# Performance work log

Hardware: AMD Instinct MI355X
Metric: run time of the kernel (lower is better)

Reference implementation:

```python
import jax, jax.numpy as jnp
import numpy as np


def setup_inputs() -> dict:
    key = jax.random.key(0)
    k1, k2 = jax.random.split(key)
    z = jax.random.normal(k1, (16, 256, 32, 32), dtype=jnp.float32)
    emb = jax.random.normal(k2, (8192, 256), dtype=jnp.float32)
    return {"z": z, "emb": emb}


def reference(z, emb):
    B, C, H, W = z.shape
    # [B,C,H,W] -> [B*H*W, C], distances in fp32 for precision
    z_f = jnp.transpose(z, (0, 2, 3, 1)).reshape(-1, C).astype(jnp.float32)
    e = emb.astype(jnp.float32)
    # squared-distance expansion: ||z||^2 - 2 z.e + ||e||^2  -> [N, K]
    d = (
        jnp.sum(z_f * z_f, axis=1, keepdims=True)
        - 2.0 * (z_f @ e.T)
        + jnp.sum(e * e, axis=1)[None, :]
    )
    idx = jnp.argmin(d, axis=1)  # [N]
    out = emb[idx].astype(z.dtype)  # codebook gather
    return jnp.transpose(out.reshape(B, H, W, C), (0, 3, 1, 2))
```

## Files before the change

kernel.cpp:

```cpp
#include <hip/hip_runtime.h>
#include <stdint.h>

#define NB   16
#define CD   256
#define HW   1024
#define NQ   16384
#define KCN  8192

typedef unsigned long long u64;
typedef unsigned short     u16;
using f32x4  = __attribute__((ext_vector_type(4))) float;
using bf16x8 = __attribute__((ext_vector_type(8))) __bf16;

#define ZTB_OFF  0
#define EMBB_OFF 8388608
#define EH_OFF   12582912
#define CAND_OFF 12615680

static __device__ __forceinline__ void gl_lds16(const void* g, void* l) {
  __builtin_amdgcn_global_load_lds(
      (const __attribute__((address_space(1))) void*)g,
      (__attribute__((address_space(3))) void*)l, 16, 0, 0);
}

static __device__ __forceinline__ unsigned bf16r(float x) {
  unsigned u = __float_as_uint(x);
  return (u + 0x7fffu + ((u >> 16) & 1u)) >> 16;
}

static __device__ __forceinline__ u64 umin64(u64 a, u64 b) { return a < b ? a : b; }
static __device__ __forceinline__ u64 umax64(u64 a, u64 b) { return a < b ? b : a; }

__global__ __launch_bounds__(256) void k_prep(const float* __restrict__ z,
                                              const float* __restrict__ emb,
                                              u16* __restrict__ zTb,
                                              u16* __restrict__ embB,
                                              float* __restrict__ eH) {
  const int bx = (int)blockIdx.x;
  if (bx < 1024) {
    __shared__ float tile[64][65];
    const int b   = bx >> 6;
    const int hwT = (bx >> 2) & 15;
    const int cT  = bx & 3;
    const int tx  = threadIdx.x & 63;
    const int ty  = threadIdx.x >> 6;
    const float* src = z + (size_t)(b * CD + cT * 64) * HW + hwT * 64;
#pragma unroll
    for (int i = 0; i < 16; ++i) {
      const int c_l = ty + 4 * i;
      tile[c_l][tx] = src[(size_t)c_l * HW + tx];
    }
    __syncthreads();
    const size_t dbase = (size_t)(b * HW + hwT * 64) * CD + cT * 64;
#pragma unroll
    for (int i = 0; i < 16; ++i) {
      const int hw_l = ty + 4 * i;
      zTb[dbase + (size_t)hw_l * CD + tx] = (u16)bf16r(tile[tx][hw_l]);
    }
  } else {
    const int wave = (bx - 1024) * 4 + ((int)threadIdx.x >> 6);
    const int lane = threadIdx.x & 63;
#pragma unroll
    for (int it = 0; it < 8; ++it) {
      const int row = wave * 8 + it;
      const float4 v = *(const float4*)(emb + (size_t)row * CD + lane * 4);
      uint2 pk;
      pk.x = bf16r(v.x) | (bf16r(v.y) << 16);
      pk.y = bf16r(v.z) | (bf16r(v.w) << 16);
      *(uint2*)(embB + (size_t)row * CD + lane * 4) = pk;
      float s = v.x * v.x + v.y * v.y + v.z * v.z + v.w * v.w;
#pragma unroll
      for (int off = 32; off; off >>= 1) s += __shfl_xor(s, off, 64);
      if (lane == 0) eH[row] = 0.5f * s + 1024.0f;
    }
  }
}


#define WAITV(N) asm volatile("s_waitcnt vmcnt(" #N ")" ::: "memory")
#define LGKM0()  asm volatile("s_waitcnt lgkmcnt(0)" ::: "memory")
#define MEMFENCE() asm volatile("" ::: "memory")

__global__ __launch_bounds__(256, 2) void k_argmin(const u16* __restrict__ zTb,
                                                   const u16* __restrict__ embB,
                                                   const float* __restrict__ eH,
                                                   u64* __restrict__ cand) {
  __shared__ __align__(16) u16 Bs[4][2][4096];

  const int tid  = (int)threadIdx.x;
  const int w    = tid >> 6;
  const int lane = tid & 63;
  const int l15  = lane & 15, quad = lane >> 4;
  const int q0    = (int)(blockIdx.x >> 3) * 128;
  const int split = (int)(blockIdx.x & 7);
  const int wq0 = (w & 1) * 64;
  const int nh  = w >> 1;

  bf16x8 Af[4][2][4];
  {
    const char* aB = (const char*)zTb + (size_t)(q0 + wq0 + l15) * 512 + quad * 16;
#pragma unroll
    for (int i = 0; i < 4; ++i)
#pragma unroll
      for (int kc = 0; kc < 2; ++kc)
#pragma unroll
        for (int ks = 0; ks < 4; ++ks)
          Af[i][kc][ks] = *(const bf16x8*)(aB + i * 8192 + kc * 256 + ks * 64);
  }
  MEMFENCE();

  char* myLds0 = (char*)&Bs[w][0][0];
  char* myLds1 = myLds0 + 8192;
  const int lane16 = lane * 16;

  const char* bW = (const char*)embB
                 + (size_t)(split * 1024 + nh * 32 + (lane >> 3)) * 512
                 + (size_t)(((lane & 7) ^ (lane >> 3)) * 16);

#define STAGE(SLOT, SRC)                                                       \
  do {                                                                         \
    const char* _s = (SRC);                                                    \
    char* _d = (SLOT) + lane16;                                                \
    gl_lds16(_s,          _d);                                                 \
    gl_lds16(_s + 4096,   _d + 1024);                                          \
    gl_lds16(_s + 8192,   _d + 2048);                                          \
    gl_lds16(_s + 12288,  _d + 3072);                                          \
    gl_lds16(_s + 128,    _d + 4096);                                          \
    gl_lds16(_s + 4224,   _d + 5120);                                          \
    gl_lds16(_s + 8320,   _d + 6144);                                          \
    gl_lds16(_s + 12416,  _d + 7168);                                          \
    MEMFENCE();                                                                \
  } while (0)

  const int gx = l15 & 7;
  const int oA = (quad ^ gx) * 16;
  const int oB = ((4 + quad) ^ gx) * 16;

  f32x4 acc[4][2];
  float b1[16], b2[16];
  const float FMAX = __uint_as_float(0x7F7FFFFFu);
#pragma unroll
  for (int s = 0; s < 16; ++s) { b1[s] = FMAX; b2[s] = FMAX; }

#define ACCZERO()                                                              \
  do {                                                                         \
    _Pragma("unroll")                                                          \
    for (int i = 0; i < 4; ++i) {                                              \
      acc[i][0] = f32x4{0.f, 0.f, 0.f, 0.f};                                   \
      acc[i][1] = f32x4{0.f, 0.f, 0.f, 0.f};                                   \
    }                                                                          \
  } while (0)

#define COMPUTE(SB, KC, ...)                                                   \
  do {                                                                         \
    const char* _sb = (const char*)(SB) + l15 * 128;                           \
    bf16x8 f00 = *(const bf16x8*)(_sb + oA);                                   \
    bf16x8 f01 = *(const bf16x8*)(_sb + 2048 + oA);                            \
    bf16x8 f10 = *(const bf16x8*)(_sb + oB);                                   \
    bf16x8 f11 = *(const bf16x8*)(_sb + 2048 + oB);                            \
    bf16x8 f20 = *(const bf16x8*)(_sb + 4096 + oA);                            \
    bf16x8 f21 = *(const bf16x8*)(_sb + 6144 + oA);                            \
    bf16x8 f30 = *(const bf16x8*)(_sb + 4096 + oB);                            \
    bf16x8 f31 = *(const bf16x8*)(_sb + 6144 + oB);                            \
    LGKM0();                                                                   \
    __VA_ARGS__;                                                               \
    __builtin_amdgcn_s_setprio(1);                                             \
    _Pragma("unroll")                                                          \
    for (int i = 0; i < 4; ++i) {                                              \
      acc[i][0] = __builtin_amdgcn_mfma_f32_16x16x32_bf16(Af[i][KC][0], f00,   \
                                                          acc[i][0], 0, 0, 0); \
      acc[i][1] = __builtin_amdgcn_mfma_f32_16x16x32_bf16(Af[i][KC][0], f01,   \
                                                          acc[i][1], 0, 0, 0); \
    }                                                                          \
    _Pragma("unroll")                                                          \
    for (int i = 0; i < 4; ++i) {                                              \
      acc[i][0] = __builtin_amdgcn_mfma_f32_16x16x32_bf16(Af[i][KC][1], f10,   \
                                                          acc[i][0], 0, 0, 0); \
      acc[i][1] = __builtin_amdgcn_mfma_f32_16x16x32_bf16(Af[i][KC][1], f11,   \
                                                          acc[i][1], 0, 0, 0); \
    }                                                                          \
    _Pragma("unroll")                                                          \
    for (int i = 0; i < 4; ++i) {                                              \
      acc[i][0] = __builtin_amdgcn_mfma_f32_16x16x32_bf16(Af[i][KC][2], f20,   \
                                                          acc[i][0], 0, 0, 0); \
      acc[i][1] = __builtin_amdgcn_mfma_f32_16x16x32_bf16(Af[i][KC][2], f21,   \
                                                          acc[i][1], 0, 0, 0); \
    }                                                                          \
    _Pragma("unroll")                                                          \
    for (int i = 0; i < 4; ++i) {                                              \
      acc[i][0] = __builtin_amdgcn_mfma_f32_16x16x32_bf16(Af[i][KC][3], f30,   \
                                                          acc[i][0], 0, 0, 0); \
      acc[i][1] = __builtin_amdgcn_mfma_f32_16x16x32_bf16(Af[i][KC][3], f31,   \
                                                          acc[i][1], 0, 0, 0); \
    }                                                                          \
    __builtin_amdgcn_s_setprio(0);                                             \
  } while (0)

#define EPILOGUE(NT, EH0, EH1)                                                 \
  do {                                                                         \
    _Pragma("unroll")                                                          \
    for (int i = 0; i < 4; ++i)                                                \
      _Pragma("unroll")                                                        \
      for (int r = 0; r < 4; ++r) {                                            \
        const int s = i * 4 + r;                                               \
        const unsigned kb0 = (__float_as_uint((EH0) - acc[i][0][r]) & ~31u)    \
                             | (unsigned)((NT) * 2 + 0);                       \
        const unsigned kb1 = (__float_as_uint((EH1) - acc[i][1][r]) & ~31u)    \
                             | (unsigned)((NT) * 2 + 1);                       \
        const float k0 = __uint_as_float(kb0), k1 = __uint_as_float(kb1);      \
        const float lo = fminf(k0, k1), hi = fmaxf(k0, k1);                    \
        b2[s] = fminf(fmaxf(lo, b1[s]), fminf(hi, b2[s]));                     \
        b1[s] = fminf(lo, b1[s]);                                              \
      }                                                                        \
  } while (0)

  const float* ehP = eH + split * 1024 + nh * 32 + l15;
  float ehA0, ehA1, ehN0 = 0.f, ehN1 = 0.f;

  const char* bC = bW;
  STAGE(myLds0, bC);
  ehA0 = ehP[0]; ehA1 = ehP[16]; MEMFENCE();
  STAGE(myLds1, bC + 256);
  const float* ehN = ehP + 64;

  for (int nt = 0; nt < 15; ++nt) {
    ACCZERO();
    WAITV(10);
    COMPUTE(myLds0, 0, STAGE(myLds0, bC + 32768));
    WAITV(8);
    COMPUTE(myLds1, 1,
            { ehN0 = ehN[0]; ehN1 = ehN[16]; MEMFENCE();
              STAGE(myLds1, bC + 32768 + 256); });
    EPILOGUE(nt, ehA0, ehA1);
    ehA0 = ehN0; ehA1 = ehN1;
    bC += 32768;
    ehN += 64;
  }

  {
    ACCZERO();
    WAITV(10);
    COMPUTE(myLds0, 0, {});
    WAITV(0);
    COMPUTE(myLds1, 1, {});
    EPILOGUE(15, ehA0, ehA1);
  }
#undef STAGE
#undef COMPUTE
#undef ACCZERO
#undef EPILOGUE

#pragma unroll
  for (int s = 0; s < 16; ++s) {
    u64 x1 = ((u64)__float_as_uint(b1[s]) << 32) | (unsigned)l15;
    u64 x2 = ((u64)__float_as_uint(b2[s]) << 32) | (unsigned)l15;
#pragma unroll
    for (int off = 1; off < 16; off <<= 1) {
      const u64 o1 = __shfl_xor(x1, off, 64);
      const u64 o2 = __shfl_xor(x2, off, 64);
      const u64 lo = umin64(x1, o1);
      const u64 hi = umax64(x1, o1);
      x1 = lo;
      x2 = umin64(hi, umin64(x2, o2));
    }
    if (l15 == 0) {
      const int i = s >> 2, r = s & 3;
      const int q = q0 + wq0 + i * 16 + quad * 4 + r;
      const unsigned kb1 = (unsigned)(x1 >> 32), kb2 = (unsigned)(x2 >> 32);
      const int id1 = (int)(kb1 & 31u), id2 = (int)(kb2 & 31u);
      const int n1 = split * 1024 + (id1 >> 1) * 64 + nh * 32
                     + (id1 & 1) * 16 + (int)(x1 & 15);
      const int n2 = split * 1024 + (id2 >> 1) * 64 + nh * 32
                     + (id2 & 1) * 16 + (int)(x2 & 15);
      cand[(size_t)q * 32 + split * 4 + nh * 2 + 0] = ((u64)kb1 << 32) | (unsigned)n1;
      cand[(size_t)q * 32 + split * 4 + nh * 2 + 1] = ((u64)kb2 << 32) | (unsigned)n2;
    }
  }
}

__global__ __launch_bounds__(256) void k_pick_out(const float* __restrict__ z,
                                                  const float* __restrict__ emb,
                                                  const u64* __restrict__ cand,
                                                  float* __restrict__ out) {
  __shared__ float zs[16][257];
  __shared__ float tile[16][257];
  const int t    = (int)threadIdx.x;
  const int lane = t & 63;
  const int wv   = t >> 6;
  const int sub  = lane >> 4;
  const int l15  = lane & 15;
  const int q0b  = (int)blockIdx.x * 16;
  const int b    = q0b >> 10, hw0 = q0b & 1023;
  const int q    = q0b + wv * 4 + sub;
  const int hwl  = wv * 4 + sub;

  {
    const float* zp = z + ((size_t)(b * CD + t)) * HW + hw0;
    const float4 a0 = *(const float4*)(zp + 0);
    const float4 a1 = *(const float4*)(zp + 4);
    const float4 a2 = *(const float4*)(zp + 8);
    const float4 a3 = *(const float4*)(zp + 12);
    zs[0][t] = a0.x;  zs[1][t] = a0.y;  zs[2][t] = a0.z;  zs[3][t] = a0.w;
    zs[4][t] = a1.x;  zs[5][t] = a1.y;  zs[6][t] = a1.z;  zs[7][t] = a1.w;
    zs[8][t] = a2.x;  zs[9][t] = a2.y;  zs[10][t] = a2.z; zs[11][t] = a2.w;
    zs[12][t] = a3.x; zs[13][t] = a3.y; zs[14][t] = a3.z; zs[15][t] = a3.w;
  }
  __syncthreads();

  const u64* cp = cand + (size_t)q * 32 + l15 * 2;
  const u64 v0 = cp[0], v1 = cp[1];
  u64 s0 = umin64(v0, v1), s1 = umax64(v0, v1), s2 = ~0ull, s3 = ~0ull;
#pragma unroll
  for (int off = 1; off < 16; off <<= 1) {
    const u64 b0 = __shfl_xor(s0, off, 64);
    const u64 b1 = __shfl_xor(s1, off, 64);
    const u64 b2 = __shfl_xor(s2, off, 64);
    const u64 b3 = __shfl_xor(s3, off, 64);
    const u64 c0 = umin64(s0, b0);
    const u64 c1 = umin64(umin64(s1, b1), umax64(s0, b0));
    const u64 c2 = umin64(umin64(s2, b2),
                          umin64(umax64(s1, b0), umax64(s0, b1)));
    const u64 c3 = umin64(umin64(umin64(s3, b3), umax64(s2, b0)),
                          umin64(umax64(s0, b2), umax64(s1, b1)));
    s0 = c0; s1 = c1; s2 = c2; s3 = c3;
  }
  const u64 sel[4] = {s0, s1, s2, s3};

  float zq[16];
#pragma unroll
  for (int j = 0; j < 16; ++j) zq[j] = zs[hwl][j * 16 + l15];

  double bd = 1e300;
  int bi = 0x7fffffff;
  float keep[16];
#pragma unroll
  for (int j = 0; j < 16; ++j) keep[j] = 0.f;
#pragma unroll
  for (int c4 = 0; c4 < 4; ++c4) {
    const int idx = (int)(unsigned)(sel[c4] & 0xffffffffull);
    const float* er = emb + (size_t)idx * CD;
    float ev[16];
#pragma unroll
    for (int j = 0; j < 16; ++j) ev[j] = er[j * 16 + l15];
    double s = 0.0;
#pragma unroll
    for (int j = 0; j < 16; ++j) {
      const double d = (double)zq[j] - (double)ev[j];
      s += d * d;
    }
#pragma unroll
    for (int off = 1; off < 16; off <<= 1) s += __shfl_xor(s, off, 64);
    const bool better = (s < bd) || (s == bd && idx < bi);
    if (better) {
      bd = s; bi = idx;
#pragma unroll
      for (int j = 0; j < 16; ++j) keep[j] = ev[j];
    }
  }
#pragma unroll
  for (int j = 0; j < 16; ++j) tile[hwl][j * 16 + l15] = keep[j];
  __syncthreads();
  const int cluster = t >> 4;
  const int ll      = t & 15;
  float* obase = out + (size_t)b * CD * HW + hw0 + ll;
#pragma unroll
  for (int j = 0; j < 16; ++j) {
    const int c = 16 * j + cluster;
    obase[(size_t)c * HW] = tile[ll][c];
  }
}

extern "C" void kernel_launch(void* const* d_in, const int* in_sizes, int n_in,
                              void* d_out, int out_size, void* d_ws, size_t ws_size,
                              hipStream_t stream) {
  const float* z   = (const float*)d_in[0];
  const float* emb = (const float*)d_in[1];
  float* out = (float*)d_out;

  char* ws = (char*)d_ws;
  u16*   zTb  = (u16*)(ws + ZTB_OFF);
  u16*   embB = (u16*)(ws + EMBB_OFF);
  float* eH   = (float*)(ws + EH_OFF);
  u64*   cand = (u64*)(ws + CAND_OFF);

  k_prep<<<1280, 256, 0, stream>>>(z, emb, zTb, embB, eH);
  k_argmin<<<1024, 256, 0, stream>>>(zTb, embB, eH, cand);
  k_pick_out<<<1024, 256, 0, stream>>>(z, emb, cand, out);
}
```

Before: 179.3 us.

## Deepen codebook LDS pipeline to a four-slot ring of half-size K chunks

Each wave's embedding staging changes from two 8 KB LDS slots, each covering 128 B of K, to a four-slot ring of 4 KB slots covering 64 B of K each. This keeps three chunks in flight while one is computed, so global-to-LDS loads overlap more of the MFMA work. The A fragments are reindexed to match the new chunking, and the explicit lgkmcnt(0) wait is dropped so the compiler handles LDS read dependencies. The cost is four times as many vmcnt waits and more fragile hand-set wait counts.

```diff
diff --git a/kernel.cpp b/kernel.cpp
--- a/kernel.cpp
+++ b/kernel.cpp
@@ -78,14 +78,13 @@
 
 
 #define WAITV(N) asm volatile("s_waitcnt vmcnt(" #N ")" ::: "memory")
-#define LGKM0()  asm volatile("s_waitcnt lgkmcnt(0)" ::: "memory")
 #define MEMFENCE() asm volatile("" ::: "memory")
 
 __global__ __launch_bounds__(256, 2) void k_argmin(const u16* __restrict__ zTb,
                                                    const u16* __restrict__ embB,
                                                    const float* __restrict__ eH,
                                                    u64* __restrict__ cand) {
-  __shared__ __align__(16) u16 Bs[4][2][4096];
+  __shared__ __align__(16) u16 Bs[4][4][2048];
 
   const int tid  = (int)threadIdx.x;
   const int w    = tid >> 6;
@@ -96,39 +95,34 @@
   const int wq0 = (w & 1) * 64;
   const int nh  = w >> 1;
 
-  bf16x8 Af[4][2][4];
+  bf16x8 Af[4][4][2];
   {
     const char* aB = (const char*)zTb + (size_t)(q0 + wq0 + l15) * 512 + quad * 16;
 #pragma unroll
     for (int i = 0; i < 4; ++i)
 #pragma unroll
-      for (int kc = 0; kc < 2; ++kc)
-#pragma unroll
-        for (int ks = 0; ks < 4; ++ks)
-          Af[i][kc][ks] = *(const bf16x8*)(aB + i * 8192 + kc * 256 + ks * 64);
+      for (int kq = 0; kq < 4; ++kq)
+#pragma unroll
+        for (int ks = 0; ks < 2; ++ks)
+          Af[i][kq][ks] = *(const bf16x8*)(aB + i * 8192 + kq * 128 + ks * 64);
   }
   MEMFENCE();
 
-  char* myLds0 = (char*)&Bs[w][0][0];
-  char* myLds1 = myLds0 + 8192;
+  char* myLds = (char*)&Bs[w][0][0];
   const int lane16 = lane * 16;
 
   const char* bW = (const char*)embB
                  + (size_t)(split * 1024 + nh * 32 + (lane >> 3)) * 512
                  + (size_t)(((lane & 7) ^ (lane >> 3)) * 16);
 
-#define STAGE(SLOT, SRC)                                                       \
+#define STAGE(SLOT_, SRC_)                                                     \
   do {                                                                         \
-    const char* _s = (SRC);                                                    \
-    char* _d = (SLOT) + lane16;                                                \
+    const char* _s = (SRC_);                                                   \
+    char* _d = myLds + (SLOT_) * 4096 + lane16;                                \
     gl_lds16(_s,          _d);                                                 \
     gl_lds16(_s + 4096,   _d + 1024);                                          \
     gl_lds16(_s + 8192,   _d + 2048);                                          \
     gl_lds16(_s + 12288,  _d + 3072);                                          \
-    gl_lds16(_s + 128,    _d + 4096);                                          \
-    gl_lds16(_s + 4224,   _d + 5120);                                          \
-    gl_lds16(_s + 8320,   _d + 6144);                                          \
-    gl_lds16(_s + 12416,  _d + 7168);                                          \
     MEMFENCE();                                                                \
   } while (0)
 
@@ -151,48 +145,31 @@
     }                                                                          \
   } while (0)
 
-#define COMPUTE(SB, KC, ...)                                                   \
+#define COMPUTE(S_, KQ_, ...)                                                  \
   do {                                                                         \
-    const char* _sb = (const char*)(SB) + l15 * 128;                           \
+    const char* _sb = myLds + (S_) * 4096 + l15 * 128;                         \
     bf16x8 f00 = *(const bf16x8*)(_sb + oA);                                   \
     bf16x8 f01 = *(const bf16x8*)(_sb + 2048 + oA);                            \
     bf16x8 f10 = *(const bf16x8*)(_sb + oB);                                   \
     bf16x8 f11 = *(const bf16x8*)(_sb + 2048 + oB);                            \
-    bf16x8 f20 = *(const bf16x8*)(_sb + 4096 + oA);                            \
-    bf16x8 f21 = *(const bf16x8*)(_sb + 6144 + oA);                            \
-    bf16x8 f30 = *(const bf16x8*)(_sb + 4096 + oB);                            \
-    bf16x8 f31 = *(const bf16x8*)(_sb + 6144 + oB);                            \
-    LGKM0();                                                                   \
     __VA_ARGS__;                                                               \
     __builtin_amdgcn_s_setprio(1);                                             \
     _Pragma("unroll")                                                          \
-    for (int i = 0; i < 4; ++i) {                                              \
-      acc[i][0] = __builtin_amdgcn_mfma_f32_16x16x32_bf16(Af[i][KC][0], f00,   \
+    for (int i = 0; i < 4; ++i)                                                \
+      acc[i][0] = __builtin_amdgcn_mfma_f32_16x16x32_bf16(Af[i][KQ_][0], f00,  \
                                                           acc[i][0], 0, 0, 0); \
-      acc[i][1] = __builtin_amdgcn_mfma_f32_16x16x32_bf16(Af[i][KC][0], f01,   \
+    _Pragma("unroll")                                                          \
+    for (int i = 0; i < 4; ++i)                                                \
+      acc[i][1] = __builtin_amdgcn_mfma_f32_16x16x32_bf16(Af[i][KQ_][0], f01,  \
                                                           acc[i][1], 0, 0, 0); \
-    }                                                                          \
-    _Pragma("unroll")                                                          \
-    for (int i = 0; i < 4; ++i) {                                              \
-      acc[i][0] = __builtin_amdgcn_mfma_f32_16x16x32_bf16(Af[i][KC][1], f10,   \
+    _Pragma("unroll")                                                          \
+    for (int i = 0; i < 4; ++i)                                                \
+      acc[i][0] = __builtin_amdgcn_mfma_f32_16x16x32_bf16(Af[i][KQ_][1], f10,  \
                                                           acc[i][0], 0, 0, 0); \
-      acc[i][1] = __builtin_amdgcn_mfma_f32_16x16x32_bf16(Af[i][KC][1], f11,   \
+    _Pragma("unroll")                                                          \
+    for (int i = 0; i < 4; ++i)                                                \
+      acc[i][1] = __builtin_amdgcn_mfma_f32_16x16x32_bf16(Af[i][KQ_][1], f11,  \
                                                           acc[i][1], 0, 0, 0); \
-    }                                                                          \
-    _Pragma("unroll")                                                          \
-    for (int i = 0; i < 4; ++i) {                                              \
-      acc[i][0] = __builtin_amdgcn_mfma_f32_16x16x32_bf16(Af[i][KC][2], f20,   \
-                                                          acc[i][0], 0, 0, 0); \
-      acc[i][1] = __builtin_amdgcn_mfma_f32_16x16x32_bf16(Af[i][KC][2], f21,   \
-                                                          acc[i][1], 0, 0, 0); \
-    }                                                                          \
-    _Pragma("unroll")                                                          \
-    for (int i = 0; i < 4; ++i) {                                              \
-      acc[i][0] = __builtin_amdgcn_mfma_f32_16x16x32_bf16(Af[i][KC][3], f30,   \
-                                                          acc[i][0], 0, 0, 0); \
-      acc[i][1] = __builtin_amdgcn_mfma_f32_16x16x32_bf16(Af[i][KC][3], f31,   \
-                                                          acc[i][1], 0, 0, 0); \
-    }                                                                          \
     __builtin_amdgcn_s_setprio(0);                                             \
   } while (0)
 
@@ -218,19 +195,20 @@
   float ehA0, ehA1, ehN0 = 0.f, ehN1 = 0.f;
 
   const char* bC = bW;
-  STAGE(myLds0, bC);
+  STAGE(0, bC);
+  STAGE(1, bC + 128);
+  STAGE(2, bC + 256);
   ehA0 = ehP[0]; ehA1 = ehP[16]; MEMFENCE();
-  STAGE(myLds1, bC + 256);
   const float* ehN = ehP + 64;
 
   for (int nt = 0; nt < 15; ++nt) {
     ACCZERO();
-    WAITV(10);
-    COMPUTE(myLds0, 0, STAGE(myLds0, bC + 32768));
-    WAITV(8);
-    COMPUTE(myLds1, 1,
-            { ehN0 = ehN[0]; ehN1 = ehN[16]; MEMFENCE();
-              STAGE(myLds1, bC + 32768 + 256); });
+    WAITV(10); COMPUTE(0, 0, STAGE(3, bC + 384));
+    WAITV(10); COMPUTE(1, 1, STAGE(0, bC + 32768));
+    WAITV(10); COMPUTE(2, 2, STAGE(1, bC + 32768 + 128));
+    WAITV(8);  COMPUTE(3, 3,
+               { STAGE(2, bC + 32768 + 256);
+                 ehN0 = ehN[0]; ehN1 = ehN[16]; MEMFENCE(); });
     EPILOGUE(nt, ehA0, ehA1);
     ehA0 = ehN0; ehA1 = ehN1;
     bC += 32768;
@@ -239,10 +217,10 @@
 
   {
     ACCZERO();
-    WAITV(10);
-    COMPUTE(myLds0, 0, {});
-    WAITV(0);
-    COMPUTE(myLds1, 1, {});
+    WAITV(10); COMPUTE(0, 0, STAGE(3, bC + 384));
+    WAITV(10); COMPUTE(1, 1, {});
+    WAITV(6);  COMPUTE(2, 2, {});
+    WAITV(0);  COMPUTE(3, 3, {});
     EPILOGUE(15, ehA0, ehA1);
   }
 #undef STAGE
```

Result: no change. 182.0 us (+1.5%).
